# Performance work log

Measured on AMD Instinct MI355X. Metric: run time of the kernel, lower is better.

Reference implementation:

```python
import jax, jax.numpy as jnp
import numpy as np
from math import sqrt

N = 50000      # n_nodes
M = 800000     # n_edges (avg degree 16)
D = 256        # d_Embedding
H = 8          # heads
DK = 32        # per-head key/query dim
DV = 32        # per-head value dim


def setup_inputs() -> dict:
    key = jax.random.key(0)
    ks = jax.random.split(key, 10)
    s = 0.02
    x = jax.random.normal(ks[0], (N, D), dtype=jnp.float32)
    edge_index = jax.random.randint(ks[1], (2, M), 0, N, dtype=jnp.int32)
    # projection weights stored pre-reshaped to (D, H, dhead); equivalent to nn.Linear(D, H*dhead)
    Wk = jax.random.normal(ks[2], (D, H, DK), dtype=jnp.float32) * s
    bk = jax.random.normal(ks[3], (H, DK), dtype=jnp.float32) * s
    Wq = jax.random.normal(ks[4], (D, H, DK), dtype=jnp.float32) * s
    bq = jax.random.normal(ks[5], (H, DK), dtype=jnp.float32) * s
    Wv = jax.random.normal(ks[6], (D, H, DV), dtype=jnp.float32) * s
    bv = jax.random.normal(ks[7], (H, DV), dtype=jnp.float32) * s
    Wagg = jax.random.normal(ks[8], (H * DV, D), dtype=jnp.float32) * s
    bagg = jnp.zeros((D,), dtype=jnp.float32)
    Wff = jax.random.normal(ks[9], (D, D), dtype=jnp.float32) * s
    bff = jnp.zeros((D,), dtype=jnp.float32)
    return {"x": x, "edge_index": edge_index, "Wk": Wk, "bk": bk, "Wq": Wq,
            "bq": bq, "Wv": Wv, "bv": bv, "Wagg": Wagg, "bagg": bagg,
            "Wff": Wff, "bff": bff}


def reference(x, edge_index, Wk, bk, Wq, bq, Wv, bv, Wagg, bagg, Wff, bff):
    recv = edge_index[0]
    send = edge_index[1]
    # per-head projections: (N, H, d)
    K = jnp.einsum('nd,dhk->nhk', x, Wk) + bk
    Q = jnp.einsum('nd,dhk->nhk', x, Wq) + bq
    V = jnp.einsum('nd,dhv->nhv', x, Wv) + bv
    # edge-wise attention logits: (M, H)
    qk = jnp.sum(Q[recv] * K[send], axis=-1)
    # faithful to original: rescale by 3/global_max, then exp
    att = jnp.exp(qk * 3.0 / jnp.max(qk))
    # segment-softmax normalization over edges sharing a receiver
    sums = jax.ops.segment_sum(att, recv, num_segments=N)  # (N, H)
    att = att / sums[recv] / sqrt(DK)
    # weighted scatter-add of sender values: (N, H, DV)
    msg = att[..., None] * V[send]
    out = jax.ops.segment_sum(msg, recv, num_segments=N)
    out = jax.nn.relu(out).reshape(N, H * DV)
    out = jax.nn.relu(out @ Wagg + bagg)
    out = jax.nn.relu(out @ Wff + bff)
    return x + out
```

## Files before the change

### kernel.cpp

```cpp
#include <hip/hip_runtime.h>

#define N_NODES 50000
#define M_EDGES 800000
#define RP 50048

typedef __bf16 bf16x8 __attribute__((ext_vector_type(8)));
typedef __bf16 bf16x4 __attribute__((ext_vector_type(4)));
typedef float  f32x4  __attribute__((ext_vector_type(4)));

static __device__ __forceinline__ unsigned enc_ord(float f) {
    unsigned b = __float_as_uint(f);
    return (b & 0x80000000u) ? ~b : (b | 0x80000000u);
}
static __device__ __forceinline__ float dec_ord(unsigned u) {
    unsigned b = (u & 0x80000000u) ? (u ^ 0x80000000u) : ~u;
    return __uint_as_float(b);
}
static __device__ __forceinline__ float bflo(unsigned u) { return __uint_as_float(u << 16); }
static __device__ __forceinline__ float bfhi(unsigned u) { return __uint_as_float(u & 0xffff0000u); }

static __device__ __forceinline__ void gload16(const void* g, void* l) {
    __builtin_amdgcn_global_load_lds(
        (const __attribute__((address_space(1))) void*)g,
        (__attribute__((address_space(3))) void*)l, 16, 0, 0);
}

__global__ __launch_bounds__(256) void prep_kernel(
    const float* __restrict__ Wk, const float* __restrict__ Wq,
    const float* __restrict__ Wv, const float* __restrict__ Wagg,
    const float* __restrict__ Wff,
    const float* __restrict__ bk, const float* __restrict__ bq,
    const float* __restrict__ bv,
    const float* __restrict__ X,
    __bf16* __restrict__ WHq, __bf16* __restrict__ WLq,
    __bf16* __restrict__ WaH, __bf16* __restrict__ WaL,
    __bf16* __restrict__ WfH, __bf16* __restrict__ WfL,
    float* __restrict__ bqkv, __bf16* __restrict__ xh, __bf16* __restrict__ xl,
    int* __restrict__ counts, int* __restrict__ cursor, unsigned* __restrict__ gmax) {
    int gid = blockIdx.x * 256 + threadIdx.x;
    int stride = gridDim.x * 256;
    for (int i = gid; i < 65536; i += stride) {
        int n = i >> 8, k = i & 255;
        size_t src = (size_t)k * 256 + n;
        float v; __bf16 h;
        v = Wk[src];   h = (__bf16)v; WHq[(size_t)n * 256 + k] = h;
                       WLq[(size_t)n * 256 + k] = (__bf16)(v - (float)h);
        v = Wq[src];   h = (__bf16)v; WHq[(size_t)(256 + n) * 256 + k] = h;
                       WLq[(size_t)(256 + n) * 256 + k] = (__bf16)(v - (float)h);
        v = Wv[src];   h = (__bf16)v; WHq[(size_t)(512 + n) * 256 + k] = h;
                       WLq[(size_t)(512 + n) * 256 + k] = (__bf16)(v - (float)h);
        v = Wagg[src]; h = (__bf16)v; WaH[i] = h; WaL[i] = (__bf16)(v - (float)h);
        v = Wff[src];  h = (__bf16)v; WfH[i] = h; WfL[i] = (__bf16)(v - (float)h);
    }
    const size_t nx = (size_t)N_NODES * 256 / 4;
    for (size_t i = gid; i < nx; i += stride) {
        float4 v = *(const float4*)(X + i * 4);
        bf16x4 hh, ll;
        hh[0] = (__bf16)v.x; ll[0] = (__bf16)(v.x - (float)hh[0]);
        hh[1] = (__bf16)v.y; ll[1] = (__bf16)(v.y - (float)hh[1]);
        hh[2] = (__bf16)v.z; ll[2] = (__bf16)(v.z - (float)hh[2]);
        hh[3] = (__bf16)v.w; ll[3] = (__bf16)(v.w - (float)hh[3]);
        *(bf16x4*)(xh + i * 4) = hh;
        *(bf16x4*)(xl + i * 4) = ll;
    }
    for (int i = gid; i < 768; i += stride)
        bqkv[i] = (i < 256) ? bk[i] : ((i < 512) ? bq[i - 256] : bv[i - 512]);
    for (int i = gid; i < N_NODES; i += stride) { counts[i] = 0; cursor[i] = 0; }
    if (gid == 0) *gmax = 0u;
}

__global__ __launch_bounds__(256) void gemm_qkv(
    const __bf16* __restrict__ Ah, const __bf16* __restrict__ Al,
    const __bf16* __restrict__ Bth, const __bf16* __restrict__ Btl,
    const float* __restrict__ bqkv,
    __bf16* __restrict__ Kb, float* __restrict__ Qo, __bf16* __restrict__ Vb) {
    __shared__ __attribute__((aligned(16))) __bf16 sm[2][4][4][128][8];

    int row0 = blockIdx.x * 128;
    int n0   = blockIdx.y * 128;
    int tid  = threadIdx.x;
    int lane = tid & 63, wave = tid >> 6;
    int wm = (wave >> 1) * 64, wn = (wave & 1) * 64;

    f32x4 acc[4][4];
    #pragma unroll
    for (int i = 0; i < 4; i++)
        #pragma unroll
        for (int j = 0; j < 4; j++) acc[i][j] = (f32x4)(0.f);

    int srow = tid & 127;
    int shi  = tid >> 7;
    const __bf16* gA0 = Ah  + (size_t)(row0 + srow) * 256;
    const __bf16* gA1 = Al  + (size_t)(row0 + srow) * 256;
    const __bf16* gB0 = Bth + (size_t)(n0 + srow) * 256;
    const __bf16* gB1 = Btl + (size_t)(n0 + srow) * 256;
    char* lds0 = (char*)&sm[0][0][0][0][0];

#define STAGE(buf, kk) do {                                                   \
        int ke0 = (kk) + shi * 8;                                             \
        int ke1 = (kk) + (2 + shi) * 8;                                       \
        size_t lo0 = (size_t)(buf) * 32768 + (size_t)tid * 16;                \
        size_t lo1 = lo0 + 4096;                                              \
        gload16(gA0 + ke0, lds0 + lo0);                                       \
        gload16(gA0 + ke1, lds0 + lo1);                                       \
        gload16(gA1 + ke0, lds0 + 8192 + lo0);                                \
        gload16(gA1 + ke1, lds0 + 8192 + lo1);                                \
        gload16(gB0 + ke0, lds0 + 16384 + lo0);                               \
        gload16(gB0 + ke1, lds0 + 16384 + lo1);                               \
        gload16(gB1 + ke0, lds0 + 24576 + lo0);                               \
        gload16(gB1 + ke1, lds0 + 24576 + lo1);                               \
    } while (0)

    STAGE(0, 0);
    __syncthreads();

    int h = lane >> 4;
    int m_base = wm + (lane & 15);
    int n_base = wn + (lane & 15);

    for (int t = 0; t < 8; t++) {
        int cur = t & 1;
        if (t < 7) STAGE(cur ^ 1, (t + 1) * 32);
        bf16x8 ahf[4], alf[4], bhf[4], blf[4];
        #pragma unroll
        for (int mt = 0; mt < 4; mt++) {
            ahf[mt] = *(const bf16x8*)&sm[cur][0][h][m_base + mt * 16][0];
            alf[mt] = *(const bf16x8*)&sm[cur][1][h][m_base + mt * 16][0];
        }
        #pragma unroll
        for (int nt = 0; nt < 4; nt++) {
            bhf[nt] = *(const bf16x8*)&sm[cur][2][h][n_base + nt * 16][0];
            blf[nt] = *(const bf16x8*)&sm[cur][3][h][n_base + nt * 16][0];
        }
        #pragma unroll
        for (int mt = 0; mt < 4; mt++)
            #pragma unroll
            for (int nt = 0; nt < 4; nt++) {
                acc[mt][nt] = __builtin_amdgcn_mfma_f32_16x16x32_bf16(ahf[mt], bhf[nt], acc[mt][nt], 0, 0, 0);
                acc[mt][nt] = __builtin_amdgcn_mfma_f32_16x16x32_bf16(alf[mt], bhf[nt], acc[mt][nt], 0, 0, 0);
                acc[mt][nt] = __builtin_amdgcn_mfma_f32_16x16x32_bf16(ahf[mt], blf[nt], acc[mt][nt], 0, 0, 0);
            }
        __syncthreads();
    }

    #pragma unroll
    for (int mt = 0; mt < 4; mt++) {
        #pragma unroll
        for (int nt = 0; nt < 4; nt++) {
            int cg = n0 + wn + nt * 16 + (lane & 15);
            #pragma unroll
            for (int rr = 0; rr < 4; rr++) {
                int row = row0 + wm + mt * 16 + (lane >> 4) * 4 + rr;
                if (row < N_NODES) {
                    float v = acc[mt][nt][rr] + bqkv[cg];
                    if (cg < 256)      Kb[(size_t)row * 256 + cg] = (__bf16)v;
                    else if (cg < 512) Qo[(size_t)row * 256 + (cg - 256)] = v;
                    else               Vb[(size_t)row * 256 + (cg - 512)] = (__bf16)v;
                }
            }
        }
    }
}

__global__ __launch_bounds__(256) void gemm_mfma(
    const __bf16* __restrict__ Ah, const __bf16* __restrict__ Al,
    const __bf16* __restrict__ Bth, const __bf16* __restrict__ Btl,
    const float* __restrict__ bias, const float* __restrict__ residual,
    float* __restrict__ C, __bf16* __restrict__ CbH, __bf16* __restrict__ CbL,
    int nrows, int do_relu) {
    __shared__ __attribute__((aligned(16))) __bf16 sm[2][4][4][128][8];

    int row0 = blockIdx.x * 128;
    int n0   = blockIdx.y * 128;
    int tid  = threadIdx.x;
    int lane = tid & 63, wave = tid >> 6;
    int wm = (wave >> 1) * 64, wn = (wave & 1) * 64;

    f32x4 acc[4][4];
    #pragma unroll
    for (int i = 0; i < 4; i++)
        #pragma unroll
        for (int j = 0; j < 4; j++) acc[i][j] = (f32x4)(0.f);

    int srow = tid & 127;
    int shi  = tid >> 7;
    const __bf16* gA0 = Ah  + (size_t)(row0 + srow) * 256;
    const __bf16* gA1 = Al  + (size_t)(row0 + srow) * 256;
    const __bf16* gB0 = Bth + (size_t)(n0 + srow) * 256;
    const __bf16* gB1 = Btl + (size_t)(n0 + srow) * 256;
    char* lds0 = (char*)&sm[0][0][0][0][0];

    STAGE(0, 0);
    __syncthreads();

    int h = lane >> 4;
    int m_base = wm + (lane & 15);
    int n_base = wn + (lane & 15);

    for (int t = 0; t < 8; t++) {
        int cur = t & 1;
        if (t < 7) STAGE(cur ^ 1, (t + 1) * 32);
        bf16x8 ahf[4], alf[4], bhf[4], blf[4];
        #pragma unroll
        for (int mt = 0; mt < 4; mt++) {
            ahf[mt] = *(const bf16x8*)&sm[cur][0][h][m_base + mt * 16][0];
            alf[mt] = *(const bf16x8*)&sm[cur][1][h][m_base + mt * 16][0];
        }
        #pragma unroll
        for (int nt = 0; nt < 4; nt++) {
            bhf[nt] = *(const bf16x8*)&sm[cur][2][h][n_base + nt * 16][0];
            blf[nt] = *(const bf16x8*)&sm[cur][3][h][n_base + nt * 16][0];
        }
        #pragma unroll
        for (int mt = 0; mt < 4; mt++)
            #pragma unroll
            for (int nt = 0; nt < 4; nt++) {
                acc[mt][nt] = __builtin_amdgcn_mfma_f32_16x16x32_bf16(ahf[mt], bhf[nt], acc[mt][nt], 0, 0, 0);
                acc[mt][nt] = __builtin_amdgcn_mfma_f32_16x16x32_bf16(alf[mt], bhf[nt], acc[mt][nt], 0, 0, 0);
                acc[mt][nt] = __builtin_amdgcn_mfma_f32_16x16x32_bf16(ahf[mt], blf[nt], acc[mt][nt], 0, 0, 0);
            }
        __syncthreads();
    }
#undef STAGE

    #pragma unroll
    for (int mt = 0; mt < 4; mt++) {
        #pragma unroll
        for (int nt = 0; nt < 4; nt++) {
            int col = n0 + wn + nt * 16 + (lane & 15);
            #pragma unroll
            for (int rr = 0; rr < 4; rr++) {
                int row = row0 + wm + mt * 16 + (lane >> 4) * 4 + rr;
                if (row < nrows) {
                    float v = acc[mt][nt][rr] + bias[col];
                    if (do_relu) v = fmaxf(v, 0.f);
                    size_t idx = (size_t)row * 256 + col;
                    if (CbH) {
                        __bf16 hh = (__bf16)v;
                        CbH[idx] = hh;
                        if (CbL) CbL[idx] = (__bf16)(v - (float)hh);
                    } else {
                        if (residual) v += residual[idx];
                        C[idx] = v;
                    }
                }
            }
        }
    }
}

__global__ void hist_kernel(const int* __restrict__ recv, int* __restrict__ counts) {
    int t = blockIdx.x * 256 + threadIdx.x;
    if (t < M_EDGES) atomicAdd(&counts[recv[t]], 1);
}

__global__ void scan_kernel(const int* __restrict__ counts, int* __restrict__ offsets) {
    __shared__ int part[256];
    int t = threadIdx.x;
    const int per = (N_NODES + 255) / 256;
    int start = t * per;
    int end = min(start + per, N_NODES);
    int s = 0;
    for (int i = start; i < end; i++) s += counts[i];
    part[t] = s;
    __syncthreads();
    if (t == 0) {
        int acc = 0;
        for (int i = 0; i < 256; i++) { int v = part[i]; part[i] = acc; acc += v; }
    }
    __syncthreads();
    int acc = part[t];
    for (int i = start; i < end; i++) { offsets[i] = acc; acc += counts[i]; }
    if (end == N_NODES && start < N_NODES) offsets[N_NODES] = acc;
}

__global__ void fill_kernel(const int* __restrict__ recv, const int* __restrict__ send,
                            const int* __restrict__ offsets,
                            int* __restrict__ cursor, int* __restrict__ ssorted,
                            int* __restrict__ rsorted) {
    int t = blockIdx.x * 256 + threadIdx.x;
    if (t < M_EDGES) {
        int r = recv[t];
        int pos = offsets[r] + atomicAdd(&cursor[r], 1);
        ssorted[pos] = send[t];
        rsorted[pos] = r;
    }
}

__global__ __launch_bounds__(256) void qk_csr_kernel(
    const int* __restrict__ ssorted, const int* __restrict__ rsorted,
    const float* __restrict__ Q, const unsigned short* __restrict__ Kb,
    float* __restrict__ qks, unsigned* __restrict__ gmax) {
    int wave_id = (blockIdx.x * 256 + threadIdx.x) >> 6;
    int lane = threadIdx.x & 63;
    int e_slot = lane >> 5;
    int sl = lane & 31;
    const int nwaves = (gridDim.x * 256) >> 6;
    const int npairs = M_EDGES / 2;
    float wmax = -INFINITY;
    for (int pp = wave_id; pp < npairs; pp += 4 * nwaves) {
        int ep[4]; bool valid[4];
        #pragma unroll
        for (int u = 0; u < 4; u++) {
            int p = pp + u * nwaves;
            valid[u] = p < npairs;
            ep[u] = (valid[u] ? p : pp) * 2 + e_slot;
        }
        int si[4], ri[4];
        #pragma unroll
        for (int u = 0; u < 4; u++) { si[u] = ssorted[ep[u]]; ri[u] = rsorted[ep[u]]; }
        uint4 kv[4]; float4 qa[4], qb[4];
        #pragma unroll
        for (int u = 0; u < 4; u++) {
            kv[u] = *(const uint4*)(Kb + (size_t)si[u] * 256 + sl * 8);
            qa[u] = *(const float4*)(Q + (size_t)ri[u] * 256 + sl * 8);
            qb[u] = *(const float4*)(Q + (size_t)ri[u] * 256 + sl * 8 + 4);
        }
        #pragma unroll
        for (int u = 0; u < 4; u++) {
            float d = qa[u].x * bflo(kv[u].x) + qa[u].y * bfhi(kv[u].x)
                    + qa[u].z * bflo(kv[u].y) + qa[u].w * bfhi(kv[u].y)
                    + qb[u].x * bflo(kv[u].z) + qb[u].y * bfhi(kv[u].z)
                    + qb[u].z * bflo(kv[u].w) + qb[u].w * bfhi(kv[u].w);
            d += __shfl_xor(d, 1);
            d += __shfl_xor(d, 2);
            wmax = fmaxf(wmax, d);
            if ((sl & 3) == 0 && valid[u])
                qks[(size_t)ep[u] * 8 + (sl >> 2)] = d;
        }
    }
    wmax = fmaxf(wmax, __shfl_xor(wmax, 1));
    wmax = fmaxf(wmax, __shfl_xor(wmax, 2));
    wmax = fmaxf(wmax, __shfl_xor(wmax, 4));
    wmax = fmaxf(wmax, __shfl_xor(wmax, 8));
    wmax = fmaxf(wmax, __shfl_xor(wmax, 16));
    wmax = fmaxf(wmax, __shfl_xor(wmax, 32));
    if (lane == 0 && wmax > -INFINITY) atomicMax(gmax, enc_ord(wmax));
}

__global__ __launch_bounds__(256) void node_agg_kernel(
    const int* __restrict__ offsets, const int* __restrict__ ssorted,
    const float* __restrict__ qks, const unsigned short* __restrict__ Vb,
    const unsigned* __restrict__ gmax,
    __bf16* __restrict__ msgH, __bf16* __restrict__ msgL) {
    int wave_id = (blockIdx.x * 256 + threadIdx.x) >> 6;
    int lane = threadIdx.x & 63;
    int h = lane >> 3;
    const int nwaves = (gridDim.x * 256) >> 6;
    const int per = (N_NODES + nwaves - 1) / nwaves;
    int n0 = wave_id * per;
    int nend = min(n0 + per, N_NODES);
    float scale = 3.0f / dec_ord(*gmax);
    for (int n = n0; n < nend; n++) {
        int off = offsets[n];
        int deg = offsets[n + 1] - off;
        float sum = 0.f, a0 = 0.f, a1 = 0.f, a2 = 0.f, a3 = 0.f;
        for (int b = 0; b < deg; b += 64) {
            int bn = min(64, deg - b);
            int idxb = ssorted[off + b + min(lane, bn - 1)];
            #define VROW(i) (*(const uint2*)(Vb + \
                (size_t)__shfl(idxb, min((i), bn - 1)) * 256 + lane * 4))
            #define QKL(i) qks[(size_t)(off + b + min((i), bn - 1)) * 8 + h]
            uint2 v0 = VROW(0);
            uint2 v1 = VROW(1);
            float q0 = QKL(0);
            float q1 = QKL(1);
            for (int i = 0; i < bn; i++) {
                uint2 vc = v0; v0 = v1; v1 = VROW(i + 2);
                float qc = q0; q0 = q1; q1 = QKL(i + 2);
                float a = __expf(qc * scale);
                sum += a;
                a0 += a * bflo(vc.x); a1 += a * bfhi(vc.x);
                a2 += a * bflo(vc.y); a3 += a * bfhi(vc.y);
            }
            #undef VROW
            #undef QKL
        }
        float inv = (deg > 0) ? 1.0f / (sum * 5.65685424949238f) : 0.f;
        float r0 = fmaxf(a0 * inv, 0.f), r1 = fmaxf(a1 * inv, 0.f);
        float r2 = fmaxf(a2 * inv, 0.f), r3 = fmaxf(a3 * inv, 0.f);
        bf16x4 hv, lv;
        hv[0] = (__bf16)r0; lv[0] = (__bf16)(r0 - (float)hv[0]);
        hv[1] = (__bf16)r1; lv[1] = (__bf16)(r1 - (float)hv[1]);
        hv[2] = (__bf16)r2; lv[2] = (__bf16)(r2 - (float)hv[2]);
        hv[3] = (__bf16)r3; lv[3] = (__bf16)(r3 - (float)hv[3]);
        *(bf16x4*)(msgH + (size_t)n * 256 + lane * 4) = hv;
        *(bf16x4*)(msgL + (size_t)n * 256 + lane * 4) = lv;
    }
}

extern "C" void kernel_launch(void* const* d_in, const int* in_sizes, int n_in,
                              void* d_out, int out_size, void* d_ws, size_t ws_size,
                              hipStream_t stream) {
    const float* x    = (const float*)d_in[0];
    const int*   edge = (const int*)d_in[1];
    const int*   recv = edge;
    const int*   send = edge + M_EDGES;
    const float* Wk   = (const float*)d_in[2];
    const float* bk   = (const float*)d_in[3];
    const float* Wq   = (const float*)d_in[4];
    const float* bq   = (const float*)d_in[5];
    const float* Wv   = (const float*)d_in[6];
    const float* bv   = (const float*)d_in[7];
    const float* Wagg = (const float*)d_in[8];
    const float* bagg = (const float*)d_in[9];
    const float* Wff  = (const float*)d_in[10];
    const float* bff  = (const float*)d_in[11];
    float* out = (float*)d_out;

    float*  Qbuf  = (float*)d_ws;
    float*  reg2  = Qbuf + (size_t)RP * 256;
    float*  qks   = reg2 + (size_t)RP * 256;
    __bf16* Kbf   = (__bf16*)(qks + (size_t)M_EDGES * 8);
    __bf16* Vbf   = Kbf + (size_t)RP * 256;
    int* counts   = (int*)(Vbf + (size_t)RP * 256);
    int* cursor   = counts + N_NODES;
    int* offsets  = cursor + N_NODES;
    int* ssorted  = offsets + N_NODES + 1;
    unsigned* gmax = (unsigned*)(ssorted + M_EDGES);
    __bf16* wt    = (__bf16*)(gmax + 1);
    __bf16* WHq = wt;
    __bf16* WLq = wt + 3 * 65536;
    __bf16* WaH = wt + 6 * 65536;  __bf16* WaL = wt + 7 * 65536;
    __bf16* WfH = wt + 8 * 65536;  __bf16* WfL = wt + 9 * 65536;
    float* bqkv = (float*)(wt + 10 * 65536);
    __bf16* xh   = (__bf16*)reg2;
    __bf16* xl   = xh + (size_t)RP * 256;
    int*    rsorted = (int*)reg2;
    __bf16* msgH = (__bf16*)reg2;
    __bf16* msgL = msgH + (size_t)RP * 256;
    __bf16* hidH = (__bf16*)Qbuf;
    __bf16* hidL = hidH + (size_t)RP * 256;

    dim3 blk(256);
    dim3 qkv_grid((N_NODES + 127) / 128, 6);
    dim3 gemm_grid((N_NODES + 127) / 128, 2);
    dim3 edge_grid((M_EDGES + 255) / 256);

    hipLaunchKernelGGL(prep_kernel, dim3(2048), blk, 0, stream,
                       Wk, Wq, Wv, Wagg, Wff, bk, bq, bv, x,
                       WHq, WLq, WaH, WaL, WfH, WfL, bqkv, xh, xl,
                       counts, cursor, gmax);
    hipLaunchKernelGGL(gemm_qkv, qkv_grid, blk, 0, stream,
                       xh, xl, WHq, WLq, bqkv, Kbf, Qbuf, Vbf);
    hipLaunchKernelGGL(hist_kernel, edge_grid, blk, 0, stream, recv, counts);
    hipLaunchKernelGGL(scan_kernel, dim3(1), blk, 0, stream, counts, offsets);
    hipLaunchKernelGGL(fill_kernel, edge_grid, blk, 0, stream, recv, send, offsets,
                       cursor, ssorted, rsorted);
    hipLaunchKernelGGL(qk_csr_kernel, dim3(1024), blk, 0, stream,
                       ssorted, rsorted, Qbuf, (const unsigned short*)Kbf, qks, gmax);
    hipLaunchKernelGGL(node_agg_kernel, dim3(2048), blk, 0, stream,
                       offsets, ssorted, qks, (const unsigned short*)Vbf, gmax,
                       msgH, msgL);
    hipLaunchKernelGGL(gemm_mfma, gemm_grid, blk, 0, stream, msgH, msgL, WaH, WaL,
                       bagg, nullptr, (float*)nullptr, hidH, hidL, N_NODES, 1);
    hipLaunchKernelGGL(gemm_mfma, gemm_grid, blk, 0, stream, hidH, hidL, WfH, WfL,
                       bff, x, out, (__bf16*)nullptr, (__bf16*)nullptr, N_NODES, 1);
}
```

Baseline: 833.5 us.

## Fuse aggregation and feed-forward GEMMs; remap QKV GEMM blocks per XCD

The two back-to-back MLP GEMMs are merged into one kernel. Each block computes a full 128x256 hidden tile in registers, packs it as split-bf16 pairs, stages it through LDS, and multiplies it by Wff before writing the residual output. This removes the hidden-activation write and re-read through global memory and one kernel launch, at the cost of much higher register pressure (two accumulator sets plus packed hidden values) and lower occupancy. The QKV GEMM also moves to a 1D grid with an XCD-aware block remapping, so adjacent column tiles of the same rows run on the same XCD and share its L2.

```diff
diff --git a/kernel.cpp b/kernel.cpp
--- a/kernel.cpp
+++ b/kernel.cpp
@@ -18,12 +18,30 @@
 }
 static __device__ __forceinline__ float bflo(unsigned u) { return __uint_as_float(u << 16); }
 static __device__ __forceinline__ float bfhi(unsigned u) { return __uint_as_float(u & 0xffff0000u); }
+static __device__ __forceinline__ unsigned short bfbits(__bf16 b) {
+    unsigned short u; __builtin_memcpy(&u, &b, 2); return u;
+}
 
 static __device__ __forceinline__ void gload16(const void* g, void* l) {
     __builtin_amdgcn_global_load_lds(
         (const __attribute__((address_space(1))) void*)g,
         (__attribute__((address_space(3))) void*)l, 16, 0, 0);
 }
+
+#define STAGE(buf, kk) do {                                                   \
+        int ke0 = (kk) + shi * 8;                                             \
+        int ke1 = (kk) + (2 + shi) * 8;                                       \
+        size_t lo0 = (size_t)(buf) * 32768 + (size_t)tid * 16;                \
+        size_t lo1 = lo0 + 4096;                                              \
+        gload16(gA0 + ke0, lds0 + lo0);                                       \
+        gload16(gA0 + ke1, lds0 + lo1);                                       \
+        gload16(gA1 + ke0, lds0 + 8192 + lo0);                                \
+        gload16(gA1 + ke1, lds0 + 8192 + lo1);                                \
+        gload16(gB0 + ke0, lds0 + 16384 + lo0);                               \
+        gload16(gB0 + ke1, lds0 + 16384 + lo1);                               \
+        gload16(gB1 + ke0, lds0 + 24576 + lo0);                               \
+        gload16(gB1 + ke1, lds0 + 24576 + lo1);                               \
+    } while (0)
 
 __global__ __launch_bounds__(256) void prep_kernel(
     const float* __restrict__ Wk, const float* __restrict__ Wq,
@@ -76,8 +94,15 @@
     __bf16* __restrict__ Kb, float* __restrict__ Qo, __bf16* __restrict__ Vb) {
     __shared__ __attribute__((aligned(16))) __bf16 sm[2][4][4][128][8];
 
-    int row0 = blockIdx.x * 128;
-    int n0   = blockIdx.y * 128;
+    const int NB = 2346, q = NB / 8, r = NB % 8;
+    int bid = blockIdx.x;
+    int xcd = bid & 7, i0 = bid >> 3;
+    int logical = (xcd < r ? xcd * (q + 1) : r * (q + 1) + (xcd - r) * q) + i0;
+    int by = logical % 6;
+    int bx = logical / 6;
+    int row0 = bx * 128;
+    int n0   = by * 128;
+
     int tid  = threadIdx.x;
     int lane = tid & 63, wave = tid >> 6;
     int wm = (wave >> 1) * 64, wn = (wave & 1) * 64;
@@ -96,21 +121,6 @@
     const __bf16* gB1 = Btl + (size_t)(n0 + srow) * 256;
     char* lds0 = (char*)&sm[0][0][0][0][0];
 
-#define STAGE(buf, kk) do {                                                   \
-        int ke0 = (kk) + shi * 8;                                             \
-        int ke1 = (kk) + (2 + shi) * 8;                                       \
-        size_t lo0 = (size_t)(buf) * 32768 + (size_t)tid * 16;                \
-        size_t lo1 = lo0 + 4096;                                              \
-        gload16(gA0 + ke0, lds0 + lo0);                                       \
-        gload16(gA0 + ke1, lds0 + lo1);                                       \
-        gload16(gA1 + ke0, lds0 + 8192 + lo0);                                \
-        gload16(gA1 + ke1, lds0 + 8192 + lo1);                                \
-        gload16(gB0 + ke0, lds0 + 16384 + lo0);                               \
-        gload16(gB0 + ke1, lds0 + 16384 + lo1);                               \
-        gload16(gB1 + ke0, lds0 + 24576 + lo0);                               \
-        gload16(gB1 + ke1, lds0 + 24576 + lo1);                               \
-    } while (0)
-
     STAGE(0, 0);
     __syncthreads();
 
@@ -156,93 +166,6 @@
                     if (cg < 256)      Kb[(size_t)row * 256 + cg] = (__bf16)v;
                     else if (cg < 512) Qo[(size_t)row * 256 + (cg - 256)] = v;
                     else               Vb[(size_t)row * 256 + (cg - 512)] = (__bf16)v;
-                }
-            }
-        }
-    }
-}
-
-__global__ __launch_bounds__(256) void gemm_mfma(
-    const __bf16* __restrict__ Ah, const __bf16* __restrict__ Al,
-    const __bf16* __restrict__ Bth, const __bf16* __restrict__ Btl,
-    const float* __restrict__ bias, const float* __restrict__ residual,
-    float* __restrict__ C, __bf16* __restrict__ CbH, __bf16* __restrict__ CbL,
-    int nrows, int do_relu) {
-    __shared__ __attribute__((aligned(16))) __bf16 sm[2][4][4][128][8];
-
-    int row0 = blockIdx.x * 128;
-    int n0   = blockIdx.y * 128;
-    int tid  = threadIdx.x;
-    int lane = tid & 63, wave = tid >> 6;
-    int wm = (wave >> 1) * 64, wn = (wave & 1) * 64;
-
-    f32x4 acc[4][4];
-    #pragma unroll
-    for (int i = 0; i < 4; i++)
-        #pragma unroll
-        for (int j = 0; j < 4; j++) acc[i][j] = (f32x4)(0.f);
-
-    int srow = tid & 127;
-    int shi  = tid >> 7;
-    const __bf16* gA0 = Ah  + (size_t)(row0 + srow) * 256;
-    const __bf16* gA1 = Al  + (size_t)(row0 + srow) * 256;
-    const __bf16* gB0 = Bth + (size_t)(n0 + srow) * 256;
-    const __bf16* gB1 = Btl + (size_t)(n0 + srow) * 256;
-    char* lds0 = (char*)&sm[0][0][0][0][0];
-
-    STAGE(0, 0);
-    __syncthreads();
-
-    int h = lane >> 4;
-    int m_base = wm + (lane & 15);
-    int n_base = wn + (lane & 15);
-
-    for (int t = 0; t < 8; t++) {
-        int cur = t & 1;
-        if (t < 7) STAGE(cur ^ 1, (t + 1) * 32);
-        bf16x8 ahf[4], alf[4], bhf[4], blf[4];
-        #pragma unroll
-        for (int mt = 0; mt < 4; mt++) {
-            ahf[mt] = *(const bf16x8*)&sm[cur][0][h][m_base + mt * 16][0];
-            alf[mt] = *(const bf16x8*)&sm[cur][1][h][m_base + mt * 16][0];
-        }
-        #pragma unroll
-        for (int nt = 0; nt < 4; nt++) {
-            bhf[nt] = *(const bf16x8*)&sm[cur][2][h][n_base + nt * 16][0];
-            blf[nt] = *(const bf16x8*)&sm[cur][3][h][n_base + nt * 16][0];
-        }
-        #pragma unroll
-        for (int mt = 0; mt < 4; mt++)
-            #pragma unroll
-            for (int nt = 0; nt < 4; nt++) {
-                acc[mt][nt] = __builtin_amdgcn_mfma_f32_16x16x32_bf16(ahf[mt], bhf[nt], acc[mt][nt], 0, 0, 0);
-                acc[mt][nt] = __builtin_amdgcn_mfma_f32_16x16x32_bf16(alf[mt], bhf[nt], acc[mt][nt], 0, 0, 0);
-                acc[mt][nt] = __builtin_amdgcn_mfma_f32_16x16x32_bf16(ahf[mt], blf[nt], acc[mt][nt], 0, 0, 0);
-            }
-        __syncthreads();
-    }
-#undef STAGE
-
-    #pragma unroll
-    for (int mt = 0; mt < 4; mt++) {
-        #pragma unroll
-        for (int nt = 0; nt < 4; nt++) {
-            int col = n0 + wn + nt * 16 + (lane & 15);
-            #pragma unroll
-            for (int rr = 0; rr < 4; rr++) {
-                int row = row0 + wm + mt * 16 + (lane >> 4) * 4 + rr;
-                if (row < nrows) {
-                    float v = acc[mt][nt][rr] + bias[col];
-                    if (do_relu) v = fmaxf(v, 0.f);
-                    size_t idx = (size_t)row * 256 + col;
-                    if (CbH) {
-                        __bf16 hh = (__bf16)v;
-                        CbH[idx] = hh;
-                        if (CbL) CbL[idx] = (__bf16)(v - (float)hh);
-                    } else {
-                        if (residual) v += residual[idx];
-                        C[idx] = v;
-                    }
                 }
             }
         }
@@ -389,6 +312,175 @@
     }
 }
 
+__global__ __launch_bounds__(256) void mlp_fused(
+    const __bf16* __restrict__ msgH, const __bf16* __restrict__ msgL,
+    const __bf16* __restrict__ WaH, const __bf16* __restrict__ WaL,
+    const __bf16* __restrict__ WfH, const __bf16* __restrict__ WfL,
+    const float* __restrict__ bagg, const float* __restrict__ bff,
+    const float* __restrict__ x, float* __restrict__ out) {
+    __shared__ __attribute__((aligned(16))) __bf16 sm[2][4][4][128][8];
+
+    int row0 = blockIdx.x * 128;
+    int tid  = threadIdx.x;
+    int lane = tid & 63, wave = tid >> 6;
+    int wm = (wave >> 1) * 64, wn = (wave & 1) * 64;
+    int srow = tid & 127;
+    int shi  = tid >> 7;
+    char* lds0 = (char*)&sm[0][0][0][0][0];
+    int h = lane >> 4;
+    int m_base = wm + (lane & 15);
+    int n_base = wn + (lane & 15);
+
+    f32x4 acc1[2][4][4];
+    #pragma unroll
+    for (int nh = 0; nh < 2; nh++)
+        #pragma unroll
+        for (int i = 0; i < 4; i++)
+            #pragma unroll
+            for (int j = 0; j < 4; j++) acc1[nh][i][j] = (f32x4)(0.f);
+
+    const __bf16* gA0 = msgH + (size_t)(row0 + srow) * 256;
+    const __bf16* gA1 = msgL + (size_t)(row0 + srow) * 256;
+    const __bf16* gB0;
+    const __bf16* gB1;
+
+    #pragma unroll
+    for (int nh = 0; nh < 2; nh++) {
+        gB0 = WaH + (size_t)(nh * 128 + srow) * 256;
+        gB1 = WaL + (size_t)(nh * 128 + srow) * 256;
+        STAGE(0, 0);
+        __syncthreads();
+        for (int t = 0; t < 8; t++) {
+            int cur = t & 1;
+            if (t < 7) STAGE(cur ^ 1, (t + 1) * 32);
+            bf16x8 ahf[4], alf[4], bhf[4], blf[4];
+            #pragma unroll
+            for (int mt = 0; mt < 4; mt++) {
+                ahf[mt] = *(const bf16x8*)&sm[cur][0][h][m_base + mt * 16][0];
+                alf[mt] = *(const bf16x8*)&sm[cur][1][h][m_base + mt * 16][0];
+            }
+            #pragma unroll
+            for (int nt = 0; nt < 4; nt++) {
+                bhf[nt] = *(const bf16x8*)&sm[cur][2][h][n_base + nt * 16][0];
+                blf[nt] = *(const bf16x8*)&sm[cur][3][h][n_base + nt * 16][0];
+            }
+            #pragma unroll
+            for (int mt = 0; mt < 4; mt++)
+                #pragma unroll
+                for (int nt = 0; nt < 4; nt++) {
+                    acc1[nh][mt][nt] = __builtin_amdgcn_mfma_f32_16x16x32_bf16(ahf[mt], bhf[nt], acc1[nh][mt][nt], 0, 0, 0);
+                    acc1[nh][mt][nt] = __builtin_amdgcn_mfma_f32_16x16x32_bf16(alf[mt], bhf[nt], acc1[nh][mt][nt], 0, 0, 0);
+                    acc1[nh][mt][nt] = __builtin_amdgcn_mfma_f32_16x16x32_bf16(ahf[mt], blf[nt], acc1[nh][mt][nt], 0, 0, 0);
+                }
+            __syncthreads();
+        }
+    }
+
+    unsigned hidp[2][4][4][4];
+    #pragma unroll
+    for (int nh = 0; nh < 2; nh++)
+        #pragma unroll
+        for (int mt = 0; mt < 4; mt++)
+            #pragma unroll
+            for (int nt = 0; nt < 4; nt++)
+                #pragma unroll
+                for (int rr = 0; rr < 4; rr++) {
+                    int col = nh * 128 + wn + nt * 16 + (lane & 15);
+                    float v = acc1[nh][mt][nt][rr] + bagg[col];
+                    v = fmaxf(v, 0.f);
+                    __bf16 hh = (__bf16)v;
+                    __bf16 hl = (__bf16)(v - (float)hh);
+                    hidp[nh][mt][nt][rr] =
+                        (unsigned)bfbits(hh) | ((unsigned)bfbits(hl) << 16);
+                }
+
+    unsigned short* chunkw = (unsigned short*)lds0;
+    const __bf16*   chunkb = (const __bf16*)lds0;
+    unsigned short* b2w    = (unsigned short*)(lds0 + 16384);
+    const __bf16*   b2b    = (const __bf16*)(lds0 + 16384);
+
+    for (int oh = 0; oh < 2; oh++) {
+        f32x4 acc2[4][4];
+        #pragma unroll
+        for (int i = 0; i < 4; i++)
+            #pragma unroll
+            for (int j = 0; j < 4; j++) acc2[i][j] = (f32x4)(0.f);
+
+        #pragma unroll
+        for (int s = 0; s < 8; s++) {
+            __syncthreads();
+            int nh = s >> 2, sq = s & 3;
+            if (wn == ((sq >= 2) ? 64 : 0)) {
+                int nt0 = (sq & 1) * 2;
+                #pragma unroll
+                for (int mt = 0; mt < 4; mt++)
+                    #pragma unroll
+                    for (int j = 0; j < 2; j++) {
+                        int nt = nt0 + j;
+                        int kc = (wn + nt * 16 + (lane & 15)) - 32 * sq;
+                        int ks = kc >> 3, e = kc & 7;
+                        #pragma unroll
+                        for (int rr = 0; rr < 4; rr++) {
+                            int row = wm + mt * 16 + (lane >> 4) * 4 + rr;
+                            unsigned u = hidp[nh][mt][nt][rr];
+                            chunkw[(size_t)ks * 1024 + row * 8 + e] =
+                                (unsigned short)(u & 0xffffu);
+                            chunkw[(size_t)(4 + ks) * 1024 + row * 8 + e] =
+                                (unsigned short)(u >> 16);
+                        }
+                    }
+            }
+            {
+                int ks0 = shi * 2;
+                #pragma unroll
+                for (int j = 0; j < 2; j++) {
+                    int ks = ks0 + j;
+                    gload16(WfH + (size_t)(oh * 128 + srow) * 256 + 32 * s + ks * 8,
+                            (char*)b2w + (size_t)ks * 2048 + srow * 16);
+                    gload16(WfL + (size_t)(oh * 128 + srow) * 256 + 32 * s + ks * 8,
+                            (char*)b2w + (size_t)(4 + ks) * 2048 + srow * 16);
+                }
+            }
+            __syncthreads();
+            bf16x8 a2h[4], a2l[4], b2h[4], b2l[4];
+            #pragma unroll
+            for (int mt = 0; mt < 4; mt++) {
+                a2h[mt] = *(const bf16x8*)&chunkb[(size_t)h * 1024 + (m_base + mt * 16) * 8];
+                a2l[mt] = *(const bf16x8*)&chunkb[(size_t)(4 + h) * 1024 + (m_base + mt * 16) * 8];
+            }
+            #pragma unroll
+            for (int nt = 0; nt < 4; nt++) {
+                b2h[nt] = *(const bf16x8*)&b2b[(size_t)h * 1024 + (n_base + nt * 16) * 8];
+                b2l[nt] = *(const bf16x8*)&b2b[(size_t)(4 + h) * 1024 + (n_base + nt * 16) * 8];
+            }
+            #pragma unroll
+            for (int mt = 0; mt < 4; mt++)
+                #pragma unroll
+                for (int nt = 0; nt < 4; nt++) {
+                    acc2[mt][nt] = __builtin_amdgcn_mfma_f32_16x16x32_bf16(a2h[mt], b2h[nt], acc2[mt][nt], 0, 0, 0);
+                    acc2[mt][nt] = __builtin_amdgcn_mfma_f32_16x16x32_bf16(a2l[mt], b2h[nt], acc2[mt][nt], 0, 0, 0);
+                    acc2[mt][nt] = __builtin_amdgcn_mfma_f32_16x16x32_bf16(a2h[mt], b2l[nt], acc2[mt][nt], 0, 0, 0);
+                }
+        }
+        #pragma unroll
+        for (int mt = 0; mt < 4; mt++)
+            #pragma unroll
+            for (int nt = 0; nt < 4; nt++) {
+                int oc = oh * 128 + wn + nt * 16 + (lane & 15);
+                #pragma unroll
+                for (int rr = 0; rr < 4; rr++) {
+                    int row = row0 + wm + mt * 16 + (lane >> 4) * 4 + rr;
+                    if (row < N_NODES) {
+                        float v = acc2[mt][nt][rr] + bff[oc];
+                        v = fmaxf(v, 0.f);
+                        size_t idx = (size_t)row * 256 + oc;
+                        out[idx] = v + x[idx];
+                    }
+                }
+            }
+    }
+}
+
 extern "C" void kernel_launch(void* const* d_in, const int* in_sizes, int n_in,
                               void* d_out, int out_size, void* d_ws, size_t ws_size,
                               hipStream_t stream) {
@@ -429,19 +521,15 @@
     int*    rsorted = (int*)reg2;
     __bf16* msgH = (__bf16*)reg2;
     __bf16* msgL = msgH + (size_t)RP * 256;
-    __bf16* hidH = (__bf16*)Qbuf;
-    __bf16* hidL = hidH + (size_t)RP * 256;
 
     dim3 blk(256);
-    dim3 qkv_grid((N_NODES + 127) / 128, 6);
-    dim3 gemm_grid((N_NODES + 127) / 128, 2);
     dim3 edge_grid((M_EDGES + 255) / 256);
 
     hipLaunchKernelGGL(prep_kernel, dim3(2048), blk, 0, stream,
                        Wk, Wq, Wv, Wagg, Wff, bk, bq, bv, x,
                        WHq, WLq, WaH, WaL, WfH, WfL, bqkv, xh, xl,
                        counts, cursor, gmax);
-    hipLaunchKernelGGL(gemm_qkv, qkv_grid, blk, 0, stream,
+    hipLaunchKernelGGL(gemm_qkv, dim3(2346), blk, 0, stream,
                        xh, xl, WHq, WLq, bqkv, Kbf, Qbuf, Vbf);
     hipLaunchKernelGGL(hist_kernel, edge_grid, blk, 0, stream, recv, counts);
     hipLaunchKernelGGL(scan_kernel, dim3(1), blk, 0, stream, counts, offsets);
@@ -452,8 +540,6 @@
     hipLaunchKernelGGL(node_agg_kernel, dim3(2048), blk, 0, stream,
                        offsets, ssorted, qks, (const unsigned short*)Vbf, gmax,
                        msgH, msgL);
-    hipLaunchKernelGGL(gemm_mfma, gemm_grid, blk, 0, stream, msgH, msgL, WaH, WaL,
-                       bagg, nullptr, (float*)nullptr, hidH, hidL, N_NODES, 1);
-    hipLaunchKernelGGL(gemm_mfma, gemm_grid, blk, 0, stream, hidH, hidL, WfH, WfL,
-                       bff, x, out, (__bf16*)nullptr, (__bf16*)nullptr, N_NODES, 1);
-}
+    hipLaunchKernelGGL(mlp_fused, dim3((N_NODES + 127) / 128), blk, 0, stream,
+                       msgH, msgL, WaH, WaL, WfH, WfL, bagg, bff, x, out);
+}
```

Result: no change. 840.3 us (+0.8%).
